# Kernel optimization log

Measured on AMD Instinct MI355X. Metric: run time of the kernel, lower is better.

The kernel has to match this reference:

```python
import jax, jax.numpy as jnp
from jax import lax
import numpy as np

B, L, E, H, PRED = 2048, 107, 128, 128, 68
NG, NL, D3 = 3, 3, 384  # 3 stacked GRUs, 3 layers each, padded input dim 3*H


def setup_inputs() -> dict:
    key = jax.random.key(0)
    ks = jax.random.split(key, 10)
    s = 0.08  # ~1/sqrt(H), matches torch GRU init scale
    return {
        "encoded_sequence": jax.random.randint(ks[0], (B, L), 0, 14),
        "encoded_structure": jax.random.randint(ks[1], (B, L), 0, 14),
        "encoded_predicted_loop_type": jax.random.randint(ks[2], (B, L), 0, 14),
        "embed_table": jax.random.normal(ks[3], (14, E), jnp.float32) * s,
        "w_ih": jax.random.normal(ks[4], (NG, NL, 2, 3 * H, D3), jnp.float32) * s,
        "w_hh": jax.random.normal(ks[5], (NG, NL, 2, 3 * H, H), jnp.float32) * s,
        "b_ih": jax.random.normal(ks[6], (NG, NL, 2, 3 * H), jnp.float32) * s,
        "b_hh": jax.random.normal(ks[7], (NG, NL, 2, 3 * H), jnp.float32) * s,
        "lin_w": jax.random.normal(ks[8], (2 * H, 3), jnp.float32) * s,
        "lin_b": jax.random.normal(ks[9], (3,), jnp.float32) * s,
    }


def _gru_dir(x, Wih, Whh, bih, bhh, reverse):
    # x: [B, L, D3]; Wih: [3H, D3]; Whh: [3H, H]. PyTorch gate order: r, z, n.
    xp = jnp.einsum('bld,gd->blg', x, Wih) + bih  # precompute input projections [B,L,3H]
    if reverse:
        xp = xp[:, ::-1]

    def step(h, xt):
        gh = h @ Whh.T + bhh  # [B, 3H]
        xr, xz, xn = jnp.split(xt, 3, axis=-1)
        hr, hz, hn = jnp.split(gh, 3, axis=-1)
        r = jax.nn.sigmoid(xr + hr)
        z = jax.nn.sigmoid(xz + hz)
        n = jnp.tanh(xn + r * hn)
        hnew = (1.0 - z) * n + z * h
        return hnew, hnew

    h0 = jnp.zeros((x.shape[0], H), x.dtype)
    _, hs = lax.scan(step, h0, jnp.swapaxes(xp, 0, 1))  # [L, B, H]
    hs = jnp.swapaxes(hs, 0, 1)
    return hs[:, ::-1] if reverse else hs


def _pad_feat(x):
    d = x.shape[-1]
    return x if d == D3 else jnp.pad(x, ((0, 0), (0, 0), (0, D3 - d)))


def reference(encoded_sequence, encoded_structure, encoded_predicted_loop_type,
              embed_table, w_ih, w_hh, b_ih, b_hh, lin_w, lin_b):
    tok = jnp.stack([encoded_sequence, encoded_structure,
                     encoded_predicted_loop_type], axis=-1)  # [B, L, 3]
    out = embed_table[tok].reshape(tok.shape[0], L, 3 * E)  # [B, L, 384]
    for g in range(NG):
        for l in range(NL):
            xin = _pad_feat(out)
            f = _gru_dir(xin, w_ih[g, l, 0], w_hh[g, l, 0], b_ih[g, l, 0], b_hh[g, l, 0], False)
            b = _gru_dir(xin, w_ih[g, l, 1], w_hh[g, l, 1], b_ih[g, l, 1], b_hh[g, l, 1], True)
            out = jnp.concatenate([f, b], axis=-1)  # [B, L, 2H]
    return out[:, :PRED] @ lin_w + lin_b  # [B, pred_len, 3]
```

## Files before the change

kernel.cpp:

```cpp
#include <hip/hip_runtime.h>
#include <hip/hip_bf16.h>

#define B_ 2048
#define L_ 107
#define E_ 128
#define H_ 128
#define PRED_ 68
#define M_ (B_*L_)

typedef __bf16 bf16;
typedef __bf16 bf16x8 __attribute__((ext_vector_type(8)));
typedef __bf16 bf16x4 __attribute__((ext_vector_type(4)));
typedef float f32x4 __attribute__((ext_vector_type(4)));

__device__ __forceinline__ float sigm(float x)  { return 1.f / (1.f + __expf(-x)); }
__device__ __forceinline__ float tanhx(float x) { return 1.f - 2.f / (1.f + __expf(2.f * x)); }

__global__ void pack_wih_k(const float* __restrict__ w_ih, bf16* __restrict__ out) {
  int idx = blockIdx.x * 256 + threadIdx.x;
  if (idx >= 9*12*6*8*64*8) return;
  int e = idx & 7;
  int lane = (idx >> 3) & 63;
  int q = idx >> 9;
  int nt = q & 7; q >>= 3;
  int nb = q % 6; q /= 6;
  int kt = q % 12; int gl = q / 12;
  int ng = nb*128 + nt*16 + (lane & 15);
  int k  = kt*32 + (lane >> 4)*8 + e;
  int d  = (ng >= 384) ? 1 : 0;
  int np = ng - d*384;
  float v = w_ih[(((size_t)(gl*2 + d)*384 + np)*384 + k)];
  out[idx] = (bf16)v;
}

__global__ void pack_whh_k(const float* __restrict__ w_hh, bf16* __restrict__ out) {
  int idx = blockIdx.x * 256 + threadIdx.x;
  if (idx >= 9*2*4*24*64*8) return;
  int e = idx & 7;
  int lane = (idx >> 3) & 63;
  int q = idx >> 9;
  int nt = q % 24; q /= 24;
  int ks = q & 3;  q >>= 2;
  int d  = q & 1;  int gl = q >> 1;
  int n = nt*16 + (lane & 15);
  int k = ks*32 + (lane >> 4)*8 + e;
  out[idx] = (bf16)w_hh[((size_t)(gl*2 + d)*384 + n)*128 + k];
}

__global__ void pack_bias_k(const float* __restrict__ b_ih, const float* __restrict__ b_hh,
                            float* __restrict__ bias, float* __restrict__ bhhn) {
  int idx = blockIdx.x * 256 + threadIdx.x;
  if (idx < 9*768) {
    int gl = idx / 768; int n = idx % 768;
    int d = (n >= 384) ? 1 : 0; int np = n - d*384;
    float v = b_ih[(gl*2 + d)*384 + np];
    if (np < 256) v += b_hh[(gl*2 + d)*384 + np];
    bias[idx] = v;
  }
  if (idx < 9*256) {
    int gl = idx / 256; int r = idx % 256;
    int d = (r >= 128) ? 1 : 0; int j = r & 127;
    bhhn[idx] = b_hh[(gl*2 + d)*384 + 256 + j];
  }
}

__global__ void shadow_k(const bf16* __restrict__ X, bf16* __restrict__ shlo,
                         bf16* __restrict__ shhi) {
  int idx = blockIdx.x * 256 + threadIdx.x;
  const int NLO = 2048*54*16;
  if (idx < NLO) {
    int k8 = idx & 15; int q = idx >> 4; int t = q % 54; int b = q / 54;
    *reinterpret_cast<bf16x8*>(shlo + ((size_t)b*54 + t)*128 + k8*8) =
      *reinterpret_cast<const bf16x8*>(X + ((size_t)b*107 + t)*256 + k8*8);
  } else {
    idx -= NLO;
    int k8 = idx & 15; int q = idx >> 4; int t = 54 + q % 53; int b = q / 53;
    if (b < 2048)
      *reinterpret_cast<bf16x8*>(shhi + ((size_t)b*53 + (t-54))*128 + k8*8) =
        *reinterpret_cast<const bf16x8*>(X + ((size_t)b*107 + t)*256 + 128 + k8*8);
  }
}

template<int L0>
__global__ __launch_bounds__(256) void gemm_proj_k(
    const bf16* __restrict__ Xin, const bf16* __restrict__ shlo, const bf16* __restrict__ shhi,
    const int* __restrict__ seq, const int* __restrict__ str, const int* __restrict__ lp,
    const float* __restrict__ table,
    const bf16* __restrict__ Bp, const float* __restrict__ bias,
    bf16* __restrict__ xpw, int len, int t0f, int t0b) {
  constexpr int KT = L0 ? 12 : 8;
  __shared__ __align__(16) bf16 TBl[L0 ? 14*136 : 8];
  __shared__ int tokl[L0 ? 3*128 : 8];
  int tid = threadIdx.x; int lane = tid & 63; int w = tid >> 6;
  int l4 = lane & 15, g4 = lane >> 4;
  int wm = w >> 1, wn = w & 1;
  int tw = blockIdx.x >> 4, mtile = blockIdx.x & 15;
  int nb = blockIdx.y, d = blockIdx.z;
  int t = d ? (t0b - tw) : (t0f + tw);

  const bf16* aLo[4]; const bf16* aHi[4];
  #pragma unroll
  for (int mt = 0; mt < 4; ++mt) {
    int b = mtile*128 + wm*64 + mt*16 + l4;
    const bf16* xr = Xin + ((size_t)b*107 + t)*256;
    if (d == 0) {
      aLo[mt] = xr;
      aHi[mt] = (t < 54) ? xr : (shhi + ((size_t)b*53 + (t-54))*128 - 128);
    } else {
      aHi[mt] = xr;
      aLo[mt] = (t < 54) ? (shlo + ((size_t)b*54 + t)*128) : xr;
    }
  }
  const bf16* Bw = Bp + (size_t)(d*3 + nb)*4096 + (size_t)(wn*4)*512 + lane*8;

  if constexpr (L0) {
    for (int i = tid; i < 1792; i += 256) TBl[(i >> 7)*136 + (i & 127)] = (bf16)table[i];
    if (tid < 128) {
      int b = mtile*128 + tid;
      int g = b*107 + t;
      tokl[tid] = seq[g]; tokl[128 + tid] = str[g]; tokl[256 + tid] = lp[g];
    }
    __syncthreads();
  }

  float bias_r[4];
  #pragma unroll
  for (int nt = 0; nt < 4; ++nt)
    bias_r[nt] = bias[d*384 + nb*128 + wn*64 + nt*16 + l4];

  f32x4 acc[4][4];
  #pragma unroll
  for (int i = 0; i < 4; ++i)
    #pragma unroll
    for (int j = 0; j < 4; ++j) { f32x4 z = {0.f,0.f,0.f,0.f}; acc[i][j] = z; }

  auto loadA = [&](bf16x8 (&dst)[4], int kt) {
    if constexpr (L0) {
      int ch = kt >> 2, kc = (kt & 3) * 32;
      #pragma unroll
      for (int mt = 0; mt < 4; ++mt)
        dst[mt] = *reinterpret_cast<const bf16x8*>(
            TBl + tokl[ch*128 + wm*64 + mt*16 + l4]*136 + kc + g4*8);
    } else {
      if (kt < 4) {
        #pragma unroll
        for (int mt = 0; mt < 4; ++mt)
          dst[mt] = *reinterpret_cast<const bf16x8*>(aLo[mt] + kt*32 + g4*8);
      } else {
        #pragma unroll
        for (int mt = 0; mt < 4; ++mt)
          dst[mt] = *reinterpret_cast<const bf16x8*>(aHi[mt] + kt*32 + g4*8);
      }
    }
  };
  auto loadB = [&](bf16x8 (&dst)[4], int kt) {
    #pragma unroll
    for (int nt = 0; nt < 4; ++nt)
      dst[nt] = *reinterpret_cast<const bf16x8*>(Bw + (size_t)kt*24576 + nt*512);
  };
  auto domfma = [&](bf16x8 (&af)[4], bf16x8 (&bfr)[4]) {
    #pragma unroll
    for (int mt = 0; mt < 4; ++mt)
      #pragma unroll
      for (int nt = 0; nt < 4; ++nt)
        acc[mt][nt] = __builtin_amdgcn_mfma_f32_16x16x32_bf16(af[mt], bfr[nt], acc[mt][nt], 0, 0, 0);
  };

  bf16x8 af0[4], bf0[4], af1[4], bf1[4];
  loadA(af0, 0); loadB(bf0, 0);
  #pragma unroll
  for (int k2 = 0; k2 < KT; k2 += 2) {
    if (k2 + 1 < KT) { loadA(af1, k2 + 1); loadB(bf1, k2 + 1); }
    domfma(af0, bf0);
    if (k2 + 2 < KT) { loadA(af0, k2 + 2); loadB(bf0, k2 + 2); }
    if (k2 + 1 < KT) domfma(af1, bf1);
  }

  int tile_m_base = tw*128 + mtile*8 + wm*4;
  int tile_n_base = nb*8 + wn*4;
  size_t dbase = d ? (size_t)len*128*24*256 : 0;
  #pragma unroll
  for (int mt = 0; mt < 4; ++mt)
    #pragma unroll
    for (int nt = 0; nt < 4; ++nt) {
      f32x4 a = acc[mt][nt]; float bv = bias_r[nt];
      bf16x4 o;
      o[0] = (bf16)(a[0] + bv); o[1] = (bf16)(a[1] + bv);
      o[2] = (bf16)(a[2] + bv); o[3] = (bf16)(a[3] + bv);
      *reinterpret_cast<bf16x4*>(xpw + dbase +
          (((size_t)(tile_m_base + mt)*24 + tile_n_base + nt) << 8) + lane*4) = o;
    }
}

__global__ __launch_bounds__(512, 1) void scan_k(const bf16* __restrict__ xpw,
                                                 const bf16* __restrict__ whh,
                                                 const float* __restrict__ bhhn,
                                                 bf16* __restrict__ xout,
                                                 float* __restrict__ hst,
                                                 int len, int t0f, int t0b, int first) {
  __shared__ __align__(16) bf16 h_lds[2][2048];
  int tid = threadIdx.x; int lane = tid & 63; int w = tid >> 6;
  int l4 = lane & 15, g4 = lane >> 4;
  int d = blockIdx.y;
  int bx = blockIdx.x;
  int b0 = bx * 16;
  const bf16* xpb = xpw + (d ? (size_t)len*128*24*256 : 0);
  int ntl[3] = { w, 8 + w, 16 + w };
  int fragoff = g4*64 + l4*4;
  int j = w*16 + l4;
  int js = j >> 5, jc3 = (j >> 3) & 3, je = j & 7;

  bf16x8 bw[3][4];
  #pragma unroll
  for (int nt = 0; nt < 3; ++nt)
    #pragma unroll
    for (int ks = 0; ks < 4; ++ks)
      bw[nt][ks] = *reinterpret_cast<const bf16x8*>(whh + ((size_t)(d*4 + ks)*24 + ntl[nt])*512 + lane*8);

  float bn = bhhn[d*128 + j];
  float h_own[4];

  if (first) {
    #pragma unroll
    for (int i = 0; i < 4; ++i) h_own[i] = 0.f;
    if (tid < 256) reinterpret_cast<float4*>(&h_lds[0][0])[tid] = make_float4(0.f, 0.f, 0.f, 0.f);
  } else {
    #pragma unroll
    for (int i = 0; i < 4; ++i) {
      h_own[i] = hst[((size_t)d*2048 + b0 + g4*4 + i)*128 + j];
      int m = g4*4 + i;
      h_lds[0][(js*64 + m + 16*jc3)*8 + je] = (bf16)h_own[i];
    }
  }

  bf16x4 xa[3], xb[3];
  {
    #pragma unroll
    for (int nt = 0; nt < 3; ++nt)
      xa[nt] = *reinterpret_cast<const bf16x4*>(xpb + (((size_t)bx*24 + ntl[nt]) << 8) + fragoff);
  }
  __syncthreads();

  auto step = [&](bf16x4 (&xu)[3], bf16x4 (&xl)[3], int tw, int pb) {
    int tc = d ? (t0b - tw) : (t0f + tw);
    int twn = (tw + 1 < len) ? (tw + 1) : (len - 1);
    bf16x8 a[4];
    #pragma unroll
    for (int ks = 0; ks < 4; ++ks)
      a[ks] = *reinterpret_cast<const bf16x8*>(&h_lds[pb][(ks*64 + lane)*8]);
    size_t tmn = (size_t)(twn*128 + bx)*24;
    #pragma unroll
    for (int nt = 0; nt < 3; ++nt)
      xl[nt] = *reinterpret_cast<const bf16x4*>(xpb + ((tmn + ntl[nt]) << 8) + fragoff);
    f32x4 acc[3];
    #pragma unroll
    for (int nt = 0; nt < 3; ++nt) { f32x4 z = {0.f,0.f,0.f,0.f}; acc[nt] = z; }
    #pragma unroll
    for (int ks = 0; ks < 4; ++ks)
      #pragma unroll
      for (int nt = 0; nt < 3; ++nt)
        acc[nt] = __builtin_amdgcn_mfma_f32_16x16x32_bf16(a[ks], bw[nt][ks], acc[nt], 0, 0, 0);
    #pragma unroll
    for (int i = 0; i < 4; ++i) {
      float r = sigm((float)xu[0][i] + acc[0][i]);
      float z = sigm((float)xu[1][i] + acc[1][i]);
      float n = tanhx((float)xu[2][i] + r * (acc[2][i] + bn));
      float hv = (1.f - z) * n + z * h_own[i];
      h_own[i] = hv;
      int m = g4*4 + i;
      h_lds[pb ^ 1][(js*64 + m + 16*jc3)*8 + je] = (bf16)hv;
    }
    __syncthreads();
    if (tid < 256) {
      int mo = tid & 15, sc = tid >> 4;
      int s = sc >> 2, c3 = sc & 3;
      bf16x8 v = *reinterpret_cast<const bf16x8*>(&h_lds[pb ^ 1][s*512 + c3*128 + mo*8]);
      *reinterpret_cast<bf16x8*>(xout + ((size_t)(b0 + mo)*107 + tc)*256 + d*128 + s*32 + c3*8) = v;
    }
  };

  for (int tw = 0; tw < len; ++tw) {
    if (tw & 1) step(xb, xa, tw, 1);
    else        step(xa, xb, tw, 0);
  }
  #pragma unroll
  for (int i = 0; i < 4; ++i)
    hst[((size_t)d*2048 + b0 + g4*4 + i)*128 + j] = h_own[i];
}

__global__ void final_k(const bf16* __restrict__ hs, const float* __restrict__ lw,
                        const float* __restrict__ lb, float* __restrict__ out) {
  __shared__ float wsm[768];
  int tid = threadIdx.x;
  for (int i = tid; i < 768; i += 256) wsm[i] = lw[i];
  __syncthreads();
  int idx = blockIdx.x * 256 + tid;
  int b = idx / 68, t = idx % 68;
  const bf16* row = hs + (size_t)(b*107 + t) * 256;
  float a0 = lb[0], a1 = lb[1], a2 = lb[2];
  for (int j0 = 0; j0 < 256; j0 += 8) {
    bf16x8 v = *reinterpret_cast<const bf16x8*>(row + j0);
    #pragma unroll
    for (int e = 0; e < 8; ++e) {
      float f = (float)v[e];
      a0 += f * wsm[(j0 + e)*3 + 0];
      a1 += f * wsm[(j0 + e)*3 + 1];
      a2 += f * wsm[(j0 + e)*3 + 2];
    }
  }
  out[(size_t)idx*3 + 0] = a0;
  out[(size_t)idx*3 + 1] = a1;
  out[(size_t)idx*3 + 2] = a2;
}

extern "C" void kernel_launch(void* const* d_in, const int* in_sizes, int n_in,
                              void* d_out, int out_size, void* d_ws, size_t ws_size,
                              hipStream_t stream) {
  const int*   seq   = (const int*)d_in[0];
  const int*   str   = (const int*)d_in[1];
  const int*   lp    = (const int*)d_in[2];
  const float* table = (const float*)d_in[3];
  const float* w_ih  = (const float*)d_in[4];
  const float* w_hh  = (const float*)d_in[5];
  const float* b_ih  = (const float*)d_in[6];
  const float* b_hh  = (const float*)d_in[7];
  const float* lw    = (const float*)d_in[8];
  const float* lb    = (const float*)d_in[9];
  float* out = (float*)d_out;
  char* ws = (char*)d_ws;

  const size_t xsz    = (size_t)M_ * 256 * 2;
  const size_t shlosz = (size_t)2048*54*128*2;
  const size_t shhisz = (size_t)2048*53*128*2;
  const size_t wihsz  = (size_t)9*12*6*8*64*8 * 2;
  const size_t whhsz  = (size_t)9*2*4*24*64*8 * 2;
  const size_t biassz = 9*768*4, bhhnsz = 9*256*4;
  const size_t hstsz  = (size_t)2*2048*128*4;
  const size_t fixed  = xsz + shlosz + shhisz + wihsz + whhsz + biassz + bhhnsz + hstsz;
  int W = 32;
  while (W > 8 && fixed + (size_t)2*2048*W*384*2 > ws_size) W -= 8;
  const size_t xpwsz = (size_t)2*2048*W*384*2;

  size_t off = 0;
  bf16* X    = (bf16*)(ws + off); off += xsz;
  bf16* XPW  = (bf16*)(ws + off); off += xpwsz;
  bf16* SHLO = (bf16*)(ws + off); off += shlosz;
  bf16* SHHI = (bf16*)(ws + off); off += shhisz;
  bf16* WIH  = (bf16*)(ws + off); off += wihsz;
  bf16* WHH  = (bf16*)(ws + off); off += whhsz;
  float* BIAS = (float*)(ws + off); off += biassz;
  float* BHHN = (float*)(ws + off); off += bhhnsz;
  float* HST  = (float*)(ws + off);

  hipLaunchKernelGGL(pack_wih_k,  dim3(2654208/256), dim3(256), 0, stream, w_ih, WIH);
  hipLaunchKernelGGL(pack_whh_k,  dim3(884736/256),  dim3(256), 0, stream, w_hh, WHH);
  hipLaunchKernelGGL(pack_bias_k, dim3(27),          dim3(256), 0, stream, b_ih, b_hh, BIAS, BHHN);

  const int phases = (107 + W - 1) / W;
  for (int gl = 0; gl < 9; ++gl) {
    if (gl != 0)
      hipLaunchKernelGGL(shadow_k, dim3(13696), dim3(256), 0, stream, X, SHLO, SHHI);
    for (int p = 0; p < phases; ++p) {
      int len = (107 - p*W < W) ? (107 - p*W) : W;
      int t0f = p*W;
      int t0b = 106 - p*W;
      if (gl == 0)
        hipLaunchKernelGGL(gemm_proj_k<1>, dim3(len*16, 3, 2), dim3(256), 0, stream,
                           X, SHLO, SHHI, seq, str, lp, table,
                           WIH + (size_t)gl*294912, BIAS + gl*768, XPW, len, t0f, t0b);
      else
        hipLaunchKernelGGL(gemm_proj_k<0>, dim3(len*16, 3, 2), dim3(256), 0, stream,
                           X, SHLO, SHHI, seq, str, lp, table,
                           WIH + (size_t)gl*294912, BIAS + gl*768, XPW, len, t0f, t0b);
      hipLaunchKernelGGL(scan_k, dim3(128, 2), dim3(512), 0, stream,
                         XPW, WHH + (size_t)gl*98304, BHHN + gl*256, X, HST,
                         len, t0f, t0b, (p == 0) ? 1 : 0);
    }
  }
  hipLaunchKernelGGL(final_k, dim3(544), dim3(256), 0, stream, X, lw, lb, out);
}
```

Measured before the change: 3.554 ms.

## Stage A tile in LDS once and loop all three N-blocks per GEMM block

The projection GEMM now loads each block's 128x256 A tile into LDS with global_load_lds (with an XOR swizzle) and reuses it across all three N-blocks in one block, instead of launching three blocks that each reread A from global memory. The hidden-state buffer X and its shadow copies are switched to a time-major [t][b] layout so each timestep's rows are contiguous for the GEMM loads and for the scan's writes. The grid shrinks by a factor of three and each block grows heavier, and the 64KB LDS use cuts per-CU occupancy, which may reduce latency hiding.

```diff
diff --git a/kernel.cpp b/kernel.cpp
--- a/kernel.cpp
+++ b/kernel.cpp
@@ -12,6 +12,12 @@
 typedef __bf16 bf16x8 __attribute__((ext_vector_type(8)));
 typedef __bf16 bf16x4 __attribute__((ext_vector_type(4)));
 typedef float f32x4 __attribute__((ext_vector_type(4)));
+
+__device__ __forceinline__ void gload16(const void* g, void* l) {
+  __builtin_amdgcn_global_load_lds(
+      (const __attribute__((address_space(1))) unsigned int*)g,
+      (__attribute__((address_space(3))) unsigned int*)l, 16, 0, 0);
+}
 
 __device__ __forceinline__ float sigm(float x)  { return 1.f / (1.f + __expf(-x)); }
 __device__ __forceinline__ float tanhx(float x) { return 1.f - 2.f / (1.f + __expf(2.f * x)); }
@@ -67,17 +73,19 @@
 __global__ void shadow_k(const bf16* __restrict__ X, bf16* __restrict__ shlo,
                          bf16* __restrict__ shhi) {
   int idx = blockIdx.x * 256 + threadIdx.x;
-  const int NLO = 2048*54*16;
+  const int NLO = 54*2048*16;
+  const int NHI = 53*2048*16;
   if (idx < NLO) {
-    int k8 = idx & 15; int q = idx >> 4; int t = q % 54; int b = q / 54;
-    *reinterpret_cast<bf16x8*>(shlo + ((size_t)b*54 + t)*128 + k8*8) =
-      *reinterpret_cast<const bf16x8*>(X + ((size_t)b*107 + t)*256 + k8*8);
+    int k8 = idx & 15; int q = idx >> 4; int b = q & 2047; int t = q >> 11;
+    *reinterpret_cast<bf16x8*>(shlo + ((size_t)t*2048 + b)*128 + k8*8) =
+      *reinterpret_cast<const bf16x8*>(X + ((size_t)t*2048 + b)*256 + k8*8);
   } else {
     idx -= NLO;
-    int k8 = idx & 15; int q = idx >> 4; int t = 54 + q % 53; int b = q / 53;
-    if (b < 2048)
-      *reinterpret_cast<bf16x8*>(shhi + ((size_t)b*53 + (t-54))*128 + k8*8) =
-        *reinterpret_cast<const bf16x8*>(X + ((size_t)b*107 + t)*256 + 128 + k8*8);
+    if (idx < NHI) {
+      int k8 = idx & 15; int q = idx >> 4; int b = q & 2047; int t = 54 + (q >> 11);
+      *reinterpret_cast<bf16x8*>(shhi + ((size_t)(t-54)*2048 + b)*128 + k8*8) =
+        *reinterpret_cast<const bf16x8*>(X + ((size_t)t*2048 + b)*256 + 128 + k8*8);
+    }
   }
 }
 
@@ -89,29 +97,15 @@
     const bf16* __restrict__ Bp, const float* __restrict__ bias,
     bf16* __restrict__ xpw, int len, int t0f, int t0b) {
   constexpr int KT = L0 ? 12 : 8;
+  __shared__ __align__(16) bf16 As[L0 ? 8 : 128*256];
   __shared__ __align__(16) bf16 TBl[L0 ? 14*136 : 8];
   __shared__ int tokl[L0 ? 3*128 : 8];
   int tid = threadIdx.x; int lane = tid & 63; int w = tid >> 6;
   int l4 = lane & 15, g4 = lane >> 4;
   int wm = w >> 1, wn = w & 1;
   int tw = blockIdx.x >> 4, mtile = blockIdx.x & 15;
-  int nb = blockIdx.y, d = blockIdx.z;
+  int d = blockIdx.y;
   int t = d ? (t0b - tw) : (t0f + tw);
-
-  const bf16* aLo[4]; const bf16* aHi[4];
-  #pragma unroll
-  for (int mt = 0; mt < 4; ++mt) {
-    int b = mtile*128 + wm*64 + mt*16 + l4;
-    const bf16* xr = Xin + ((size_t)b*107 + t)*256;
-    if (d == 0) {
-      aLo[mt] = xr;
-      aHi[mt] = (t < 54) ? xr : (shhi + ((size_t)b*53 + (t-54))*128 - 128);
-    } else {
-      aHi[mt] = xr;
-      aLo[mt] = (t < 54) ? (shlo + ((size_t)b*54 + t)*128) : xr;
-    }
-  }
-  const bf16* Bw = Bp + (size_t)(d*3 + nb)*4096 + (size_t)(wn*4)*512 + lane*8;
 
   if constexpr (L0) {
     for (int i = tid; i < 1792; i += 256) TBl[(i >> 7)*136 + (i & 127)] = (bf16)table[i];
@@ -121,75 +115,95 @@
       tokl[tid] = seq[g]; tokl[128 + tid] = str[g]; tokl[256 + tid] = lp[g];
     }
     __syncthreads();
-  }
-
-  float bias_r[4];
+  } else {
+    #pragma unroll
+    for (int i = 0; i < 16; ++i) {
+      int id = tid + 256*i;
+      int r = id >> 5, cs = id & 31;
+      int sc = (cs & ~3) | ((cs & 3) ^ ((r >> 1) & 3));
+      int bg = mtile*128 + r;
+      const bf16* xr = Xin + ((size_t)t*2048 + bg)*256;
+      const bf16* src;
+      if (sc < 16) {
+        src = (d == 0) ? xr
+              : ((t < 54) ? (shlo + ((size_t)t*2048 + bg)*128) : xr);
+      } else {
+        src = (d == 0) ? ((t < 54) ? xr : (shhi + ((size_t)(t-54)*2048 + bg)*128 - 128))
+              : xr;
+      }
+      gload16(src + sc*8, As + (size_t)id*8);
+    }
+    __syncthreads();
+  }
+
+  float bias_r[3][4];
   #pragma unroll
-  for (int nt = 0; nt < 4; ++nt)
-    bias_r[nt] = bias[d*384 + nb*128 + wn*64 + nt*16 + l4];
-
-  f32x4 acc[4][4];
-  #pragma unroll
-  for (int i = 0; i < 4; ++i)
-    #pragma unroll
-    for (int j = 0; j < 4; ++j) { f32x4 z = {0.f,0.f,0.f,0.f}; acc[i][j] = z; }
-
-  auto loadA = [&](bf16x8 (&dst)[4], int kt) {
+  for (int nb = 0; nb < 3; ++nb)
+    #pragma unroll
+    for (int nt = 0; nt < 4; ++nt)
+      bias_r[nb][nt] = bias[d*384 + nb*128 + wn*64 + nt*16 + l4];
+
+  auto loadB = [&](bf16x8 (&dst)[4], int nb, int kt) {
+    #pragma unroll
+    for (int nt = 0; nt < 4; ++nt)
+      dst[nt] = *reinterpret_cast<const bf16x8*>(
+          Bp + (((size_t)(kt*6 + d*3 + nb)*8 + wn*4 + nt) << 9) + lane*8);
+  };
+  auto loadA = [&](bf16x8 (&af)[4], int kt) {
     if constexpr (L0) {
       int ch = kt >> 2, kc = (kt & 3) * 32;
       #pragma unroll
       for (int mt = 0; mt < 4; ++mt)
-        dst[mt] = *reinterpret_cast<const bf16x8*>(
+        af[mt] = *reinterpret_cast<const bf16x8*>(
             TBl + tokl[ch*128 + wm*64 + mt*16 + l4]*136 + kc + g4*8);
     } else {
-      if (kt < 4) {
+      #pragma unroll
+      for (int mt = 0; mt < 4; ++mt) {
+        int r = wm*64 + mt*16 + l4;
+        int cs = kt*4 + (g4 ^ ((r >> 1) & 3));
+        af[mt] = *reinterpret_cast<const bf16x8*>(As + (size_t)(r*32 + cs)*8);
+      }
+    }
+  };
+
+  int tile_m_base = tw*128 + mtile*8 + wm*4;
+  size_t dbase = d ? (size_t)len*128*24*256 : 0;
+
+  bf16x8 bf0[4], bf1[4], af[4];
+  loadB(bf0, 0, 0);
+  #pragma unroll
+  for (int nb = 0; nb < 3; ++nb) {
+    f32x4 acc[4][4];
+    #pragma unroll
+    for (int i = 0; i < 4; ++i)
+      #pragma unroll
+      for (int j = 0; j < 4; ++j) { f32x4 z = {0.f,0.f,0.f,0.f}; acc[i][j] = z; }
+    #pragma unroll
+    for (int kt = 0; kt < KT; ++kt) {
+      if (kt + 1 < KT)      loadB(bf1, nb, kt + 1);
+      else if (nb + 1 < 3)  loadB(bf1, nb + 1, 0);
+      loadA(af, kt);
+      #pragma unroll
+      for (int mt = 0; mt < 4; ++mt)
         #pragma unroll
-        for (int mt = 0; mt < 4; ++mt)
-          dst[mt] = *reinterpret_cast<const bf16x8*>(aLo[mt] + kt*32 + g4*8);
-      } else {
-        #pragma unroll
-        for (int mt = 0; mt < 4; ++mt)
-          dst[mt] = *reinterpret_cast<const bf16x8*>(aHi[mt] + kt*32 + g4*8);
+        for (int nt = 0; nt < 4; ++nt)
+          acc[mt][nt] = __builtin_amdgcn_mfma_f32_16x16x32_bf16(af[mt], bf0[nt], acc[mt][nt], 0, 0, 0);
+      #pragma unroll
+      for (int q = 0; q < 4; ++q) bf0[q] = bf1[q];
+    }
+    int tile_n_base = nb*8 + wn*4;
+    #pragma unroll
+    for (int mt = 0; mt < 4; ++mt)
+      #pragma unroll
+      for (int nt = 0; nt < 4; ++nt) {
+        f32x4 a = acc[mt][nt]; float bv = bias_r[nb][nt];
+        bf16x4 o;
+        o[0] = (bf16)(a[0] + bv); o[1] = (bf16)(a[1] + bv);
+        o[2] = (bf16)(a[2] + bv); o[3] = (bf16)(a[3] + bv);
+        *reinterpret_cast<bf16x4*>(xpw + dbase +
+            (((size_t)(tile_m_base + mt)*24 + tile_n_base + nt) << 8) + lane*4) = o;
       }
-    }
-  };
-  auto loadB = [&](bf16x8 (&dst)[4], int kt) {
-    #pragma unroll
-    for (int nt = 0; nt < 4; ++nt)
-      dst[nt] = *reinterpret_cast<const bf16x8*>(Bw + (size_t)kt*24576 + nt*512);
-  };
-  auto domfma = [&](bf16x8 (&af)[4], bf16x8 (&bfr)[4]) {
-    #pragma unroll
-    for (int mt = 0; mt < 4; ++mt)
-      #pragma unroll
-      for (int nt = 0; nt < 4; ++nt)
-        acc[mt][nt] = __builtin_amdgcn_mfma_f32_16x16x32_bf16(af[mt], bfr[nt], acc[mt][nt], 0, 0, 0);
-  };
-
-  bf16x8 af0[4], bf0[4], af1[4], bf1[4];
-  loadA(af0, 0); loadB(bf0, 0);
-  #pragma unroll
-  for (int k2 = 0; k2 < KT; k2 += 2) {
-    if (k2 + 1 < KT) { loadA(af1, k2 + 1); loadB(bf1, k2 + 1); }
-    domfma(af0, bf0);
-    if (k2 + 2 < KT) { loadA(af0, k2 + 2); loadB(bf0, k2 + 2); }
-    if (k2 + 1 < KT) domfma(af1, bf1);
-  }
-
-  int tile_m_base = tw*128 + mtile*8 + wm*4;
-  int tile_n_base = nb*8 + wn*4;
-  size_t dbase = d ? (size_t)len*128*24*256 : 0;
-  #pragma unroll
-  for (int mt = 0; mt < 4; ++mt)
-    #pragma unroll
-    for (int nt = 0; nt < 4; ++nt) {
-      f32x4 a = acc[mt][nt]; float bv = bias_r[nt];
-      bf16x4 o;
-      o[0] = (bf16)(a[0] + bv); o[1] = (bf16)(a[1] + bv);
-      o[2] = (bf16)(a[2] + bv); o[3] = (bf16)(a[3] + bv);
-      *reinterpret_cast<bf16x4*>(xpw + dbase +
-          (((size_t)(tile_m_base + mt)*24 + tile_n_base + nt) << 8) + lane*4) = o;
-    }
+  }
 }
 
 __global__ __launch_bounds__(512, 1) void scan_k(const bf16* __restrict__ xpw,
@@ -275,7 +289,7 @@
       int mo = tid & 15, sc = tid >> 4;
       int s = sc >> 2, c3 = sc & 3;
       bf16x8 v = *reinterpret_cast<const bf16x8*>(&h_lds[pb ^ 1][s*512 + c3*128 + mo*8]);
-      *reinterpret_cast<bf16x8*>(xout + ((size_t)(b0 + mo)*107 + tc)*256 + d*128 + s*32 + c3*8) = v;
+      *reinterpret_cast<bf16x8*>(xout + ((size_t)tc*2048 + b0 + mo)*256 + d*128 + s*32 + c3*8) = v;
     }
   };
 
@@ -296,7 +310,7 @@
   __syncthreads();
   int idx = blockIdx.x * 256 + tid;
   int b = idx / 68, t = idx % 68;
-  const bf16* row = hs + (size_t)(b*107 + t) * 256;
+  const bf16* row = hs + ((size_t)t*2048 + b) * 256;
   float a0 = lb[0], a1 = lb[1], a2 = lb[2];
   for (int j0 = 0; j0 < 256; j0 += 8) {
     bf16x8 v = *reinterpret_cast<const bf16x8*>(row + j0);
@@ -330,8 +344,8 @@
   char* ws = (char*)d_ws;
 
   const size_t xsz    = (size_t)M_ * 256 * 2;
-  const size_t shlosz = (size_t)2048*54*128*2;
-  const size_t shhisz = (size_t)2048*53*128*2;
+  const size_t shlosz = (size_t)54*2048*128*2;
+  const size_t shhisz = (size_t)53*2048*128*2;
   const size_t wihsz  = (size_t)9*12*6*8*64*8 * 2;
   const size_t whhsz  = (size_t)9*2*4*24*64*8 * 2;
   const size_t biassz = 9*768*4, bhhnsz = 9*256*4;
@@ -365,11 +379,11 @@
       int t0f = p*W;
       int t0b = 106 - p*W;
       if (gl == 0)
-        hipLaunchKernelGGL(gemm_proj_k<1>, dim3(len*16, 3, 2), dim3(256), 0, stream,
+        hipLaunchKernelGGL(gemm_proj_k<1>, dim3(len*16, 2), dim3(256), 0, stream,
                            X, SHLO, SHHI, seq, str, lp, table,
                            WIH + (size_t)gl*294912, BIAS + gl*768, XPW, len, t0f, t0b);
       else
-        hipLaunchKernelGGL(gemm_proj_k<0>, dim3(len*16, 3, 2), dim3(256), 0, stream,
+        hipLaunchKernelGGL(gemm_proj_k<0>, dim3(len*16, 2), dim3(256), 0, stream,
                            X, SHLO, SHHI, seq, str, lp, table,
                            WIH + (size_t)gl*294912, BIAS + gl*768, XPW, len, t0f, t0b);
       hipLaunchKernelGGL(scan_k, dim3(128, 2), dim3(512), 0, stream,
```

New measurement: 2.962 ms. 16.7% less time.
